# Kernel tuning notes

Measured on AMD Instinct MI355X. Metric: run time of the kernel, lower is better.

Reference implementation:

```python
import jax, jax.numpy as jnp
import numpy as np

LM_TEMP = 2.0      # opts.lm_temp
LAMBDA_SH = 20.0   # lambda_sh passed in ot_loss
EPS = 1e-8


def sinkhorn(M, a, b, lam, num_iter_max=1000, stop_thr=0.005):
    """Faithful port of sinkhorn_pytorch. M:[S,V], a:[S,B], b:[V,B]."""
    K = jnp.exp(-M * lam)          # [S,V]
    KM = K * M
    u0 = jnp.ones_like(a) / a.shape[0]
    v0 = jnp.zeros_like(b)

    def cond(state):
        cpt, u, v, err = state
        return (cpt < num_iter_max) & (err > stop_thr)

    def body(state):
        cpt, u, v, err = state
        u = a / (K @ (b / (u.T @ K).T))   # fused fixed-point step
        cpt = cpt + 1
        do_check = ((cpt % 20) == 1) | (cpt == num_iter_max)

        def check(uve):
            u, v, _ = uve
            v = b / (K.T @ u)
            u = a / (K @ v)
            bb = v * (K.T @ u)
            err = jnp.max(jnp.sum(jnp.abs(bb - b), axis=0))  # inf-norm over batch
            return u, v, err

        u, v, err = jax.lax.cond(do_check, check, lambda t: t, (u, v, err))
        return cpt, u, v, err

    state0 = (jnp.asarray(0, jnp.int32), u0, v0, jnp.asarray(1.0, M.dtype))
    _, u, v, _ = jax.lax.while_loop(cond, body, state0)
    return jnp.sum(u * (KM @ v), axis=0)   # [B] sinkhorn divergences


def setup_inputs() -> dict:
    key = jax.random.key(0)
    ks = jax.random.split(key, 6)
    B, H, V, NV, MAX_SLOTS = 512, 1024, 28996, 3000, 33
    inputs = jax.random.normal(ks[0], (B, 2 * H), jnp.float32)
    outputs = jax.random.normal(ks[1], (B, 512), jnp.float32)
    W_lm = jax.random.normal(ks[2], (V, H), jnp.float32) * 0.02   # lm head (no bias)
    W_lin = jax.random.normal(ks[3], (MAX_SLOTS, 512), jnp.float32) * 0.05
    b_lin = jnp.zeros((MAX_SLOTS,), jnp.float32)
    topics = jax.random.normal(ks[4], (MAX_SLOTS - 1, H), jnp.float32) * 0.01
    verbs = jax.random.randint(ks[5], (NV,), 0, V)
    return {"inputs": inputs, "outputs": outputs, "W_lm": W_lm,
            "W_lin": W_lin, "b_lin": b_lin, "topics": topics,
            "verbs": verbs, "nslots": 33}


def reference(inputs, outputs, W_lm, W_lin, b_lin, topics, verbs, nslots):
    H = W_lm.shape[1]
    # gather verb rows of the lm head once: logits[:, verbs] == x @ W_lm[verbs].T
    W_v = W_lm[verbs]                               # [NV, H]
    Wt = W_v.T                                      # [H, NV]
    o11 = jax.nn.softmax((inputs[:, :H] @ Wt) / LM_TEMP, axis=-1)
    o12 = jax.nn.softmax((inputs[:, H:] @ Wt) / LM_TEMP, axis=-1)
    o1 = (o11 + o12) * 0.5
    o1 = o1 / jnp.sum(o1, axis=1, keepdims=True)    # [B, NV] vocab marginals
    o2 = jax.nn.softmax((outputs @ W_lin.T + b_lin)[:, 1:nslots], axis=-1)  # [B, S]
    # cosine-distance cost matrix between topics and verb embeddings
    tn = topics[:nslots - 1]
    tn = tn / (jnp.linalg.norm(tn, axis=1, keepdims=True) + EPS)
    vn = W_v / (jnp.linalg.norm(W_v, axis=1, keepdims=True) + EPS)
    M = 1.0 - tn @ vn.T                             # [S, NV]
    # single chunk of ot_loss (B <= 1024): mean sinkhorn divergence
    return jnp.mean(sinkhorn(M, o2.T, o1.T, LAMBDA_SH))
```

## Files before the change

kernel.cpp:

```cpp
#include <hip/hip_runtime.h>

#define NV 3000
#define HH 1024
#define BB 512

typedef __attribute__((ext_vector_type(8))) short short8;
typedef __attribute__((ext_vector_type(4))) float floatx4;

__device__ __forceinline__ float wave_sum(float x) {
#pragma unroll
  for (int off = 32; off; off >>= 1) x += __shfl_xor(x, off, 64);
  return x;
}
__device__ __forceinline__ unsigned bf16r(float x) {
  unsigned u = __float_as_uint(x);
  u += 0x7fffu + ((u >> 16) & 1u);
  return u >> 16;
}
__device__ __forceinline__ void gload16(const void* g, void* l) {
  __builtin_amdgcn_global_load_lds(
      (const __attribute__((address_space(1))) unsigned*)g,
      (__attribute__((address_space(3))) unsigned*)l, 16, 0, 0);
}

__global__ __launch_bounds__(256) void norms_wb_kernel(
    const float* __restrict__ W_lm, const float* __restrict__ topics,
    const int* __restrict__ verbs, float* __restrict__ vninv,
    float* __restrict__ tninv, unsigned short* __restrict__ Wb) {
  int r = blockIdx.x, t = threadIdx.x;
  bool isW = r < 3072;
  int j = isW ? (r < NV ? r : NV - 1) : 0;
  const float* src = isW ? (W_lm + (size_t)verbs[j] * HH)
                         : (topics + (size_t)(r - 3072) * HH);
  float4 v = *(const float4*)(src + t * 4);
  if (isW) {
    *(uint2*)(Wb + (size_t)r * HH + t * 4) =
        make_uint2(bf16r(v.x) | (bf16r(v.y) << 16),
                   bf16r(v.z) | (bf16r(v.w) << 16));
  }
  float ss = v.x * v.x + v.y * v.y + v.z * v.z + v.w * v.w;
  ss = wave_sum(ss);
  __shared__ float sq[4];
  if ((t & 63) == 0) sq[t >> 6] = ss;
  __syncthreads();
  if (t == 0) {
    float inv = 1.0f / (sqrtf(sq[0] + sq[1] + sq[2] + sq[3]) + 1e-8f);
    if (isW) { if (r < NV) vninv[r] = inv; }
    else tninv[r - 3072] = inv;
  }
}

__global__ __launch_bounds__(256) void xb_kernel(
    const float* __restrict__ inputs, unsigned short* __restrict__ Xb) {
  int idx = blockIdx.x * 256 + threadIdx.x;
  int r = idx >> 7, c8 = (idx & 127) << 3;
  const float* src = (r < 512) ? (inputs + (size_t)r * 2048 + c8)
                               : (inputs + (size_t)(r - 512) * 2048 + 1024 + c8);
  float4 x0 = ((const float4*)src)[0];
  float4 x1 = ((const float4*)src)[1];
  uint4 o;
  o.x = bf16r(x0.x) | (bf16r(x0.y) << 16);
  o.y = bf16r(x0.z) | (bf16r(x0.w) << 16);
  o.z = bf16r(x1.x) | (bf16r(x1.y) << 16);
  o.w = bf16r(x1.z) | (bf16r(x1.w) << 16);
  *(uint4*)(Xb + (size_t)r * HH + c8) = o;
}

__global__ __launch_bounds__(256) void topt_kernel(
    const float* __restrict__ topics, const float* __restrict__ tninv,
    float* __restrict__ topT) {
  int idx = blockIdx.x * 256 + threadIdx.x;
  int k = idx >> 5, s = idx & 31;
  topT[idx] = topics[(size_t)s * HH + k] * tninv[s];
}

__global__ __launch_bounds__(64) void a_kernel(
    const float* __restrict__ outputs, const float* __restrict__ W_lin,
    const float* __restrict__ b_lin, float* __restrict__ aT) {
  int r = blockIdx.x, t = threadIdx.x;
  __shared__ float orow[512];
  __shared__ float lg[33];
  __shared__ float ms[2];
  *(float4*)(orow + t * 8)     = *(const float4*)(outputs + (size_t)r * 512 + t * 8);
  *(float4*)(orow + t * 8 + 4) = *(const float4*)(outputs + (size_t)r * 512 + t * 8 + 4);
  __syncthreads();
  if (t < 33) {
    float acc = b_lin[t];
    for (int k = 0; k < 512; ++k) acc = fmaf(orow[k], W_lin[(size_t)t * 512 + k], acc);
    lg[t] = acc;
  }
  __syncthreads();
  if (t == 0) {
    float m = lg[1];
    for (int i = 2; i < 33; ++i) m = fmaxf(m, lg[i]);
    float ssum = 0.0f;
    for (int i = 1; i < 33; ++i) ssum += __expf(lg[i] - m);
    ms[0] = m; ms[1] = ssum;
  }
  __syncthreads();
  if (t >= 1 && t < 33) aT[(size_t)r * 32 + t - 1] = __expf(lg[t] - ms[0]) / ms[1];
}

__global__ __launch_bounds__(256) void gemm_mfma(
    const unsigned short* __restrict__ Xb, const unsigned short* __restrict__ Wb,
    float* __restrict__ L) {
  __shared__ unsigned short As[128 * 32], Bs[128 * 32];
  int t = threadIdx.x;
  int wave = t >> 6, ln = t & 63;
  int bn = blockIdx.x, bm = blockIdx.y;
  int wm = (wave >> 1) * 64, wn = (wave & 1) * 64;
  const unsigned short* ga = Xb + (size_t)(bm * 128 + (t >> 2)) * HH + (t & 3) * 8;
  const unsigned short* gb = Wb + (size_t)(bn * 128 + (t >> 2)) * HH + (t & 3) * 8;
  int lq = ln >> 4, lm = ln & 15;
  floatx4 acc[4][4];
#pragma unroll
  for (int i = 0; i < 4; ++i)
#pragma unroll
    for (int j = 0; j < 4; ++j) acc[i][j] = (floatx4)0.0f;

  for (int k0 = 0; k0 < HH; k0 += 32) {
    __syncthreads();
    gload16(ga + k0, As + t * 8);
    gload16(ga + (size_t)64 * HH + k0, As + 2048 + t * 8);
    gload16(gb + k0, Bs + t * 8);
    gload16(gb + (size_t)64 * HH + k0, Bs + 2048 + t * 8);
    __syncthreads();
    short8 af[4], bfr[4];
#pragma unroll
    for (int i = 0; i < 4; ++i)
      af[i] = *(const short8*)(As + (wm + i * 16 + lm) * 32 + lq * 8);
#pragma unroll
    for (int j = 0; j < 4; ++j)
      bfr[j] = *(const short8*)(Bs + (wn + j * 16 + lm) * 32 + lq * 8);
#pragma unroll
    for (int i = 0; i < 4; ++i)
#pragma unroll
      for (int j = 0; j < 4; ++j)
        acc[i][j] = __builtin_amdgcn_mfma_f32_16x16x32_bf16(af[i], bfr[j], acc[i][j], 0, 0, 0);
  }
  int row0 = bm * 128 + wm + lq * 4;
  int col0 = bn * 128 + wn + lm;
#pragma unroll
  for (int j = 0; j < 4; ++j) {
    int col = col0 + j * 16;
    if (col < NV) {
#pragma unroll
      for (int i = 0; i < 4; ++i) {
#pragma unroll
        for (int r = 0; r < 4; ++r)
          L[(size_t)(row0 + i * 16 + r) * NV + col] = acc[i][j][r] * 0.5f;
      }
    }
  }
}

__global__ __launch_bounds__(256) void softmax_kernel(
    float* __restrict__ L1, const float* __restrict__ L2) {
  int r = blockIdx.x, t = threadIdx.x, w = t >> 6, ln = t & 63;
  float* row1 = L1 + (size_t)r * NV;
  const float* row2 = L2 + (size_t)r * NV;
  __shared__ float rd[2][4];
  float s1 = 0.0f, s2 = 0.0f;
  for (int v = t; v < NV; v += 256) { s1 += __expf(row1[v]); s2 += __expf(row2[v]); }
  s1 = wave_sum(s1); s2 = wave_sum(s2);
  if (ln == 0) { rd[0][w] = s1; rd[1][w] = s2; }
  __syncthreads();
  s1 = rd[0][0] + rd[0][1] + rd[0][2] + rd[0][3];
  s2 = rd[1][0] + rd[1][1] + rd[1][2] + rd[1][3];
  float i1 = 0.5f / s1, i2 = 0.5f / s2;
  float rs = 0.0f;
  for (int v = t; v < NV; v += 256) {
    float o = __expf(row1[v]) * i1 + __expf(row2[v]) * i2;
    row1[v] = o; rs += o;
  }
  rs = wave_sum(rs);
  __syncthreads();
  if (ln == 0) rd[0][w] = rs;
  __syncthreads();
  float rinv = 1.0f / (rd[0][0] + rd[0][1] + rd[0][2] + rd[0][3]);
  for (int v = t; v < NV; v += 256) row1[v] *= rinv;
}

__global__ __launch_bounds__(256) void mk_kernel(
    const float* __restrict__ W_lm, const int* __restrict__ verbs,
    const float* __restrict__ topT, const float* __restrict__ vninv,
    unsigned* __restrict__ Kb, float* __restrict__ KMt) {
  __shared__ float red[4][64][33];
  int t = threadIdx.x, ln = t & 63, w = t >> 6;
  int v = blockIdx.x * 64 + ln;
  int vc = v < NV ? v : NV - 1;
  int kb = __builtin_amdgcn_readfirstlane(w) << 8;
  const float* wrow = W_lm + (size_t)verbs[vc] * HH + kb;
  const float* tb = topT + (size_t)kb * 32;
  float acc[32];
#pragma unroll
  for (int s = 0; s < 32; ++s) acc[s] = 0.0f;
  for (int kk = 0; kk < 256; kk += 4) {
    float4 w4 = *(const float4*)(wrow + kk);
    const float* tr = tb + kk * 32;
    const float* pw = (const float*)&w4;
#pragma unroll
    for (int d = 0; d < 4; ++d)
#pragma unroll
      for (int s = 0; s < 32; ++s) acc[s] = fmaf(pw[d], tr[d * 32 + s], acc[s]);
  }
#pragma unroll
  for (int s = 0; s < 32; ++s) red[w][ln][s] = acc[s];
  __syncthreads();
  for (int idx = t; idx < 1024; idx += 256) {
    int l = idx >> 4, pr = idx & 15;
    int vo = blockIdx.x * 64 + l;
    if (vo < NV) {
      int s0 = pr * 2, s1 = s0 + 1;
      float vi = vninv[vo];
      float d0 = red[0][l][s0] + red[1][l][s0] + red[2][l][s0] + red[3][l][s0];
      float d1 = red[0][l][s1] + red[1][l][s1] + red[2][l][s1] + red[3][l][s1];
      float M0 = 1.0f - d0 * vi, M1 = 1.0f - d1 * vi;
      float K0 = __expf(-20.0f * M0), K1 = __expf(-20.0f * M1);
      *(float2*)(KMt + (size_t)vo * 32 + s0) = make_float2(K0 * M0, K1 * M1);
      Kb[(size_t)vo * 16 + pr] = bf16r(K0) | (bf16r(K1) << 16);
    }
  }
}

__device__ __forceinline__ void gridbar(unsigned* bar, unsigned target) {
  __syncthreads();
  if (threadIdx.x == 0) {
    __hip_atomic_fetch_add(bar, 1u, __ATOMIC_RELEASE, __HIP_MEMORY_SCOPE_AGENT);
    while (__hip_atomic_load(bar, __ATOMIC_ACQUIRE, __HIP_MEMORY_SCOPE_AGENT) < target) {
      __builtin_amdgcn_s_sleep(1);
    }
  }
  __syncthreads();
}

#define UNPK(q, o)                                          \
  kc[(o) + 0] = __uint_as_float((q).x << 16);               \
  kc[(o) + 1] = __uint_as_float((q).x & 0xffff0000u);       \
  kc[(o) + 2] = __uint_as_float((q).y << 16);               \
  kc[(o) + 3] = __uint_as_float((q).y & 0xffff0000u);       \
  kc[(o) + 4] = __uint_as_float((q).z << 16);               \
  kc[(o) + 5] = __uint_as_float((q).z & 0xffff0000u);       \
  kc[(o) + 6] = __uint_as_float((q).w << 16);               \
  kc[(o) + 7] = __uint_as_float((q).w & 0xffff0000u);

template <bool STORE_T>
__device__ __forceinline__ void kpass_ss(
    const uint4* __restrict__ Kb, const float* __restrict__ bsh0,
    const float* __restrict__ bsh1, const float* u0, const float* u1,
    float* z0, float* z1, float* vsh0, float* vsh1, int pid, int p) {
#pragma unroll 3
  for (int i = 0; i < 6; ++i) {
    int v = pid + (i << 9);
    if (i < 5 || v < NV) {
      const uint4* kq = Kb + ((size_t)v << 2) + (p << 1);
      uint4 q0 = kq[0], q1 = kq[1];
      float kc[16];
      UNPK(q0, 0) UNPK(q1, 8)
      float w0 = 0.0f, w1 = 0.0f;
#pragma unroll
      for (int s = 0; s < 16; ++s) { w0 = fmaf(kc[s], u0[s], w0); w1 = fmaf(kc[s], u1[s], w1); }
      w0 += __shfl_xor(w0, 1, 64);
      w1 += __shfl_xor(w1, 1, 64);
      float t0 = bsh0[v] * __builtin_amdgcn_rcpf(w0);
      float t1 = bsh1[v] * __builtin_amdgcn_rcpf(w1);
      if (STORE_T && !p) { vsh0[v] = t0; vsh1[v] = t1; }
#pragma unroll
      for (int s = 0; s < 16; ++s) { z0[s] = fmaf(kc[s], t0, z0[s]); z1[s] = fmaf(kc[s], t1, z1[s]); }
    }
  }
}

__device__ __forceinline__ void errpass_ss(
    const uint4* __restrict__ Kb, const float* __restrict__ bsh0,
    const float* __restrict__ bsh1, const float* u0, const float* u1,
    const float* vsh0, const float* vsh1, float& ep0, float& ep1,
    int pid, int p) {
#pragma unroll 3
  for (int i = 0; i < 6; ++i) {
    int v = pid + (i << 9);
    if (i < 5 || v < NV) {
      const uint4* kq = Kb + ((size_t)v << 2) + (p << 1);
      uint4 q0 = kq[0], q1 = kq[1];
      float kc[16];
      UNPK(q0, 0) UNPK(q1, 8)
      float w0 = 0.0f, w1 = 0.0f;
#pragma unroll
      for (int s = 0; s < 16; ++s) { w0 = fmaf(kc[s], u0[s], w0); w1 = fmaf(kc[s], u1[s], w1); }
      w0 += __shfl_xor(w0, 1, 64);
      w1 += __shfl_xor(w1, 1, 64);
      if (!p) {
        ep0 += fabsf(vsh0[v] * w0 - bsh0[v]);
        ep1 += fabsf(vsh1[v] * w1 - bsh1[v]);
      }
    }
  }
}

__device__ __forceinline__ float waveRS16(float* z, int ln) {
  int cnt = 16;
#pragma unroll
  for (int d = 2; d <= 16; d <<= 1) {
    int half = cnt >> 1;
    bool hi = (ln & d) != 0;
#pragma unroll
    for (int k = 0; k < 8; ++k) {
      if (k < half) {
        float a = z[k], b = z[half + k];
        z[k] = hi ? b : a;
        z[half + k] = hi ? a : b;
      }
    }
#pragma unroll
    for (int k = 0; k < 8; ++k)
      if (k < half) z[k] += __shfl_xor(z[half + k], d, 64);
    cnt = half;
  }
  return z[0] + __shfl_xor(z[0], 32, 64);
}

__global__ __launch_bounds__(1024) void sinkhorn_kernel(
    const uint4* __restrict__ Kb, const float* __restrict__ KMt,
    const float* __restrict__ bT, const float* __restrict__ aT,
    unsigned* __restrict__ slots, float* __restrict__ outp) {
  const int t = threadIdx.x;
  const int w = t >> 6, ln = t & 63;
  const int p = t & 1, pid = t >> 1;
  const int col0 = blockIdx.x << 1;
  const float* b0r = bT + (size_t)col0 * NV;
  const float* b1r = b0r + NV;
  float* accres = (float*)(slots + 64);
  unsigned* bar = slots + 65;

  __shared__ float zred[2][16][32];
  __shared__ float ush[2][32];
  __shared__ float sredA[16], sredB[16];
  __shared__ unsigned ebits;
  __shared__ float vsh0[3072], vsh1[3072];
  __shared__ float bsh0[3072], bsh1[3072];
  float* ushf = &ush[0][0];

  const int sl = ((ln & 1) << 4) | ((ln & 2) << 2) | (ln & 4) |
                 ((ln & 8) >> 2) | ((ln & 16) >> 4);

  for (int idx = t; idx < NV; idx += 1024) { bsh0[idx] = b0r[idx]; bsh1[idx] = b1r[idx]; }
  float areg = (t < 64) ? aT[(size_t)col0 * 32 + t] : 0.0f;

  float u0[16], u1[16];
#pragma unroll
  for (int s = 0; s < 16; ++s) { u0[s] = 1.0f / 32.0f; u1[s] = 1.0f / 32.0f; }
  if (t < 64) ushf[t] = 1.0f / 32.0f;
  __syncthreads();
  float err = 1.0f;
  int cpt = 0, chk = 0;
  unsigned barcnt = 0;

  while (cpt < 1000 && err > 0.005f) {
    float z0[16], z1[16];
#pragma unroll
    for (int s = 0; s < 16; ++s) { z0[s] = 0.0f; z1[s] = 0.0f; }
    kpass_ss<false>(Kb, bsh0, bsh1, u0, u1, z0, z1, vsh0, vsh1, pid, p);
    float r0 = waveRS16(z0, ln), r1 = waveRS16(z1, ln);
    __syncthreads();
    if (ln < 32) { zred[0][w][sl] = r0; zred[1][w][sl] = r1; }
    __syncthreads();
    if (t < 64) {
      int c = t >> 5, s = t & 31;
      float zz = 0.0f;
#pragma unroll
      for (int k = 0; k < 16; ++k) zz += zred[c][k][s];
      ushf[t] = areg * __builtin_amdgcn_rcpf(zz);
    }
    __syncthreads();
#pragma unroll
    for (int q = 0; q < 4; ++q) {
      *(float4*)(u0 + q * 4) = *(float4*)(&ush[0][(p << 4) + q * 4]);
      *(float4*)(u1 + q * 4) = *(float4*)(&ush[1][(p << 4) + q * 4]);
    }
    ++cpt;

    if (cpt % 20 == 1 || cpt == 1000) {
#pragma unroll
      for (int s = 0; s < 16; ++s) { z0[s] = 0.0f; z1[s] = 0.0f; }
      kpass_ss<true>(Kb, bsh0, bsh1, u0, u1, z0, z1, vsh0, vsh1, pid, p);
      r0 = waveRS16(z0, ln); r1 = waveRS16(z1, ln);
      __syncthreads();
      if (ln < 32) { zred[0][w][sl] = r0; zred[1][w][sl] = r1; }
      __syncthreads();
      if (t < 64) {
        int c = t >> 5, s = t & 31;
        float zz = 0.0f;
#pragma unroll
        for (int k = 0; k < 16; ++k) zz += zred[c][k][s];
        ushf[t] = areg * __builtin_amdgcn_rcpf(zz);
      }
      __syncthreads();
#pragma unroll
      for (int q = 0; q < 4; ++q) {
        *(float4*)(u0 + q * 4) = *(float4*)(&ush[0][(p << 4) + q * 4]);
        *(float4*)(u1 + q * 4) = *(float4*)(&ush[1][(p << 4) + q * 4]);
      }
      float ep0 = 0.0f, ep1 = 0.0f;
      errpass_ss(Kb, bsh0, bsh1, u0, u1, vsh0, vsh1, ep0, ep1, pid, p);
      ep0 = wave_sum(ep0); ep1 = wave_sum(ep1);
      if (ln == 0) { sredA[w] = ep0; sredB[w] = ep1; }
      __syncthreads();
      if (t == 0) {
        float e0 = 0.0f, e1 = 0.0f;
#pragma unroll
        for (int k = 0; k < 16; ++k) { e0 += sredA[k]; e1 += sredB[k]; }
        atomicMax(slots + chk, __float_as_uint(fmaxf(e0, e1)));
      }
      ++barcnt;
      gridbar(bar, barcnt * 256u);
      if (t == 0) ebits = __hip_atomic_load(slots + chk, __ATOMIC_RELAXED, __HIP_MEMORY_SCOPE_AGENT);
      __syncthreads();
      err = __uint_as_float(ebits);
      ++chk;
    }
  }

  float y0[16], y1[16];
#pragma unroll
  for (int s = 0; s < 16; ++s) { y0[s] = 0.0f; y1[s] = 0.0f; }
#pragma unroll 3
  for (int i = 0; i < 6; ++i) {
    int v = pid + (i << 9);
    if (i < 5 || v < NV) {
      const float4* kp = (const float4*)(KMt + (size_t)v * 32 + (p << 4));
      float kc[16];
#pragma unroll
      for (int q = 0; q < 4; ++q) *(float4*)(kc + q * 4) = kp[q];
      float x0 = vsh0[v], x1 = vsh1[v];
#pragma unroll
      for (int s = 0; s < 16; ++s) { y0[s] = fmaf(kc[s], x0, y0[s]); y1[s] = fmaf(kc[s], x1, y1[s]); }
    }
  }
  float r0 = waveRS16(y0, ln), r1 = waveRS16(y1, ln);
  __syncthreads();
  if (ln < 32) { zred[0][w][sl] = r0; zred[1][w][sl] = r1; }
  __syncthreads();
  if (t < 64) {
    int c = t >> 5, s = t & 31;
    float ys = 0.0f;
#pragma unroll
    for (int k = 0; k < 16; ++k) ys += zred[c][k][s];
    float pp = ys * ushf[t];
#pragma unroll
    for (int off = 1; off <= 16; off <<= 1) pp += __shfl_xor(pp, off, 64);
    float other = __shfl_xor(pp, 32, 64);
    if (t == 0) atomicAdd(accres, pp + other);
  }
  ++barcnt;
  gridbar(bar, barcnt * 256u);
  if (blockIdx.x == 0 && t == 0) {
    unsigned ab = __hip_atomic_load((unsigned*)accres, __ATOMIC_RELAXED, __HIP_MEMORY_SCOPE_AGENT);
    outp[0] = __uint_as_float(ab) / 512.0f;
  }
}

extern "C" void kernel_launch(void* const* d_in, const int* in_sizes, int n_in,
                              void* d_out, int out_size, void* d_ws, size_t ws_size,
                              hipStream_t stream) {
  (void)in_sizes; (void)n_in; (void)out_size; (void)ws_size;
  const float* inputs  = (const float*)d_in[0];
  const float* outputs = (const float*)d_in[1];
  const float* W_lm    = (const float*)d_in[2];
  const float* W_lin   = (const float*)d_in[3];
  const float* b_lin   = (const float*)d_in[4];
  const float* topics  = (const float*)d_in[5];
  const int*   verbs   = (const int*)d_in[6];
  float* out = (float*)d_out;

  char* ws = (char*)d_ws;
  float*    L     = (float*)(ws);
  float*    L1    = L;
  float*    L2    = (float*)(ws + 6144000);
  float*    aT    = (float*)(ws + 12288000);
  unsigned* Kb    = (unsigned*)(ws + 12353536);
  float*    KMt   = (float*)(ws + 12545536);
  float*    topT  = (float*)(ws + 12929536);
  float*    vninv = (float*)(ws + 13060608);
  float*    tninv = (float*)(ws + 13072640);
  unsigned* slots = (unsigned*)(ws + 13072768);
  unsigned short* Xb = (unsigned short*)(ws + 13073280);
  unsigned short* Wb = (unsigned short*)(ws + 15170432);

  hipMemsetAsync((void*)slots, 0, 512, stream);

  norms_wb_kernel<<<3104, 256, 0, stream>>>(W_lm, topics, verbs, vninv, tninv, Wb);
  xb_kernel<<<512, 256, 0, stream>>>(inputs, Xb);
  topt_kernel<<<128, 256, 0, stream>>>(topics, tninv, topT);
  a_kernel<<<BB, 64, 0, stream>>>(outputs, W_lin, b_lin, aT);
  gemm_mfma<<<dim3(24, 8), 256, 0, stream>>>(Xb, Wb, L);
  softmax_kernel<<<BB, 256, 0, stream>>>(L1, L2);
  mk_kernel<<<47, 256, 0, stream>>>(W_lm, verbs, topT, vninv, Kb, KMt);
  sinkhorn_kernel<<<256, 1024, 0, stream>>>((const uint4*)Kb, KMt, L1, aT, slots, out);
}
```

Before: 413.6 us.

## Run Sinkhorn matvecs on bf16 MFMA with split hi/lo vectors

Replaces the scalar FMA K·u and K^T·v passes in the persistent Sinkhorn kernel with 16x16x32 bf16 MFMA instructions. A transposed padded copy of K is added, and the u and v vectors are split into bf16 high and low parts to keep precision close to fp32. The b rows are now read from global memory each iteration instead of being cached in LDS. This aims to cut the vector ALU cost of each iteration, at the cost of extra LDS traffic, more block barriers and some precision risk.

```diff
diff --git a/kernel.cpp b/kernel.cpp
--- a/kernel.cpp
+++ b/kernel.cpp
@@ -184,7 +184,8 @@
 __global__ __launch_bounds__(256) void mk_kernel(
     const float* __restrict__ W_lm, const int* __restrict__ verbs,
     const float* __restrict__ topT, const float* __restrict__ vninv,
-    unsigned* __restrict__ Kb, float* __restrict__ KMt) {
+    unsigned* __restrict__ Kb, unsigned short* __restrict__ KbT,
+    float* __restrict__ KMt) {
   __shared__ float red[4][64][33];
   int t = threadIdx.x, ln = t & 63, w = t >> 6;
   int v = blockIdx.x * 64 + ln;
@@ -210,15 +211,22 @@
   for (int idx = t; idx < 1024; idx += 256) {
     int l = idx >> 4, pr = idx & 15;
     int vo = blockIdx.x * 64 + l;
+    int s0 = pr * 2, s1 = s0 + 1;
     if (vo < NV) {
-      int s0 = pr * 2, s1 = s0 + 1;
       float vi = vninv[vo];
       float d0 = red[0][l][s0] + red[1][l][s0] + red[2][l][s0] + red[3][l][s0];
       float d1 = red[0][l][s1] + red[1][l][s1] + red[2][l][s1] + red[3][l][s1];
       float M0 = 1.0f - d0 * vi, M1 = 1.0f - d1 * vi;
       float K0 = __expf(-20.0f * M0), K1 = __expf(-20.0f * M1);
       *(float2*)(KMt + (size_t)vo * 32 + s0) = make_float2(K0 * M0, K1 * M1);
-      Kb[(size_t)vo * 16 + pr] = bf16r(K0) | (bf16r(K1) << 16);
+      unsigned b0 = bf16r(K0), b1 = bf16r(K1);
+      Kb[(size_t)vo * 16 + pr] = b0 | (b1 << 16);
+      KbT[(size_t)s0 * 3008 + vo] = (unsigned short)b0;
+      KbT[(size_t)s1 * 3008 + vo] = (unsigned short)b1;
+    } else {
+      Kb[(size_t)vo * 16 + pr] = 0u;
+      KbT[(size_t)s0 * 3008 + vo] = 0;
+      KbT[(size_t)s1 * 3008 + vo] = 0;
     }
   }
 }
@@ -232,69 +240,6 @@
     }
   }
   __syncthreads();
-}
-
-#define UNPK(q, o)                                          \
-  kc[(o) + 0] = __uint_as_float((q).x << 16);               \
-  kc[(o) + 1] = __uint_as_float((q).x & 0xffff0000u);       \
-  kc[(o) + 2] = __uint_as_float((q).y << 16);               \
-  kc[(o) + 3] = __uint_as_float((q).y & 0xffff0000u);       \
-  kc[(o) + 4] = __uint_as_float((q).z << 16);               \
-  kc[(o) + 5] = __uint_as_float((q).z & 0xffff0000u);       \
-  kc[(o) + 6] = __uint_as_float((q).w << 16);               \
-  kc[(o) + 7] = __uint_as_float((q).w & 0xffff0000u);
-
-template <bool STORE_T>
-__device__ __forceinline__ void kpass_ss(
-    const uint4* __restrict__ Kb, const float* __restrict__ bsh0,
-    const float* __restrict__ bsh1, const float* u0, const float* u1,
-    float* z0, float* z1, float* vsh0, float* vsh1, int pid, int p) {
-#pragma unroll 3
-  for (int i = 0; i < 6; ++i) {
-    int v = pid + (i << 9);
-    if (i < 5 || v < NV) {
-      const uint4* kq = Kb + ((size_t)v << 2) + (p << 1);
-      uint4 q0 = kq[0], q1 = kq[1];
-      float kc[16];
-      UNPK(q0, 0) UNPK(q1, 8)
-      float w0 = 0.0f, w1 = 0.0f;
-#pragma unroll
-      for (int s = 0; s < 16; ++s) { w0 = fmaf(kc[s], u0[s], w0); w1 = fmaf(kc[s], u1[s], w1); }
-      w0 += __shfl_xor(w0, 1, 64);
-      w1 += __shfl_xor(w1, 1, 64);
-      float t0 = bsh0[v] * __builtin_amdgcn_rcpf(w0);
-      float t1 = bsh1[v] * __builtin_amdgcn_rcpf(w1);
-      if (STORE_T && !p) { vsh0[v] = t0; vsh1[v] = t1; }
-#pragma unroll
-      for (int s = 0; s < 16; ++s) { z0[s] = fmaf(kc[s], t0, z0[s]); z1[s] = fmaf(kc[s], t1, z1[s]); }
-    }
-  }
-}
-
-__device__ __forceinline__ void errpass_ss(
-    const uint4* __restrict__ Kb, const float* __restrict__ bsh0,
-    const float* __restrict__ bsh1, const float* u0, const float* u1,
-    const float* vsh0, const float* vsh1, float& ep0, float& ep1,
-    int pid, int p) {
-#pragma unroll 3
-  for (int i = 0; i < 6; ++i) {
-    int v = pid + (i << 9);
-    if (i < 5 || v < NV) {
-      const uint4* kq = Kb + ((size_t)v << 2) + (p << 1);
-      uint4 q0 = kq[0], q1 = kq[1];
-      float kc[16];
-      UNPK(q0, 0) UNPK(q1, 8)
-      float w0 = 0.0f, w1 = 0.0f;
-#pragma unroll
-      for (int s = 0; s < 16; ++s) { w0 = fmaf(kc[s], u0[s], w0); w1 = fmaf(kc[s], u1[s], w1); }
-      w0 += __shfl_xor(w0, 1, 64);
-      w1 += __shfl_xor(w1, 1, 64);
-      if (!p) {
-        ep0 += fabsf(vsh0[v] * w0 - bsh0[v]);
-        ep1 += fabsf(vsh1[v] * w1 - bsh1[v]);
-      }
-    }
-  }
 }
 
 __device__ __forceinline__ float waveRS16(float* z, int ln) {
@@ -320,11 +265,13 @@
 }
 
 __global__ __launch_bounds__(1024) void sinkhorn_kernel(
-    const uint4* __restrict__ Kb, const float* __restrict__ KMt,
-    const float* __restrict__ bT, const float* __restrict__ aT,
-    unsigned* __restrict__ slots, float* __restrict__ outp) {
+    const unsigned short* __restrict__ Kb, const unsigned short* __restrict__ KbT,
+    const float* __restrict__ KMt, const float* __restrict__ bT,
+    const float* __restrict__ aT, unsigned* __restrict__ slots,
+    float* __restrict__ outp) {
   const int t = threadIdx.x;
-  const int w = t >> 6, ln = t & 63;
+  const int wv = t >> 6, ln = t & 63;
+  const int lm = ln & 15, lq = ln >> 4;
   const int p = t & 1, pid = t >> 1;
   const int col0 = blockIdx.x << 1;
   const float* b0r = bT + (size_t)col0 * NV;
@@ -332,78 +279,149 @@
   float* accres = (float*)(slots + 64);
   unsigned* bar = slots + 65;
 
-  __shared__ float zred[2][16][32];
-  __shared__ float ush[2][32];
+  __shared__ __align__(16) float wshp0[3008], wshp1[3008];
+  __shared__ __align__(16) unsigned short wtbuf[4][3008];
+  __shared__ __align__(16) float zred[16][2][32];
+  __shared__ float ushf[64];
+  __shared__ __align__(16) unsigned short ub[4][32];
   __shared__ float sredA[16], sredB[16];
   __shared__ unsigned ebits;
-  __shared__ float vsh0[3072], vsh1[3072];
-  __shared__ float bsh0[3072], bsh1[3072];
-  float* ushf = &ush[0][0];
+
+  float* wlo0 = (float*)&wtbuf[0][0];
+  float* wlo1 = (float*)&wtbuf[2][0];
+  float* wbase = (lm == 0) ? wshp0 : (lm == 1) ? wshp1 : (lm == 2) ? wlo0 : wlo1;
+  const unsigned short* zbsel = &wtbuf[lm & 3][0];
+  const unsigned short* ubsel = &ub[lm & 3][0];
 
   const int sl = ((ln & 1) << 4) | ((ln & 2) << 2) | (ln & 4) |
                  ((ln & 8) >> 2) | ((ln & 16) >> 4);
 
-  for (int idx = t; idx < NV; idx += 1024) { bsh0[idx] = b0r[idx]; bsh1[idx] = b1r[idx]; }
   float areg = (t < 64) ? aT[(size_t)col0 * 32 + t] : 0.0f;
-
-  float u0[16], u1[16];
-#pragma unroll
-  for (int s = 0; s < 16; ++s) { u0[s] = 1.0f / 32.0f; u1[s] = 1.0f / 32.0f; }
-  if (t < 64) ushf[t] = 1.0f / 32.0f;
-  __syncthreads();
+  if (t < 64) {
+    int c = t >> 5, s = t & 31;
+    ushf[t] = 1.0f / 32.0f;
+    ub[c][s] = (unsigned short)0x3D00u;
+    ub[2 + c][s] = 0;
+  }
+  __syncthreads();
+
   float err = 1.0f;
   int cpt = 0, chk = 0;
   unsigned barcnt = 0;
 
-  while (cpt < 1000 && err > 0.005f) {
-    float z0[16], z1[16];
-#pragma unroll
-    for (int s = 0; s < 16; ++s) { z0[s] = 0.0f; z1[s] = 0.0f; }
-    kpass_ss<false>(Kb, bsh0, bsh1, u0, u1, z0, z1, vsh0, vsh1, pid, p);
-    float r0 = waveRS16(z0, ln), r1 = waveRS16(z1, ln);
-    __syncthreads();
-    if (ln < 32) { zred[0][w][sl] = r0; zred[1][w][sl] = r1; }
+  auto full_iter = [&]() {
+    {
+      short8 bfu = *(const short8*)(ubsel + (lq << 3));
+#pragma unroll
+      for (int i = 0; i < 12; ++i) {
+        int c = wv + (i << 4);
+        if (c < 188) {
+          int v0 = c << 4;
+          short8 af = *(const short8*)(Kb + (size_t)(v0 + lm) * 32 + (lq << 3));
+          floatx4 acc = (floatx4)0.0f;
+          acc = __builtin_amdgcn_mfma_f32_16x16x32_bf16(af, bfu, acc, 0, 0, 0);
+          if (lm < 4) *(floatx4*)(wbase + v0 + (lq << 2)) = acc;
+        }
+      }
+    }
+    __syncthreads();
+    float t0r[3], t1r[3];
+#pragma unroll
+    for (int i = 0; i < 3; ++i) {
+      int v = t + (i << 10);
+      t0r[i] = 0.0f; t1r[i] = 0.0f;
+      if (v < NV) {
+        float w0 = wshp0[v] + wlo0[v];
+        float w1 = wshp1[v] + wlo1[v];
+        t0r[i] = b0r[v] * __builtin_amdgcn_rcpf(w0);
+        t1r[i] = b1r[v] * __builtin_amdgcn_rcpf(w1);
+      }
+    }
+    __syncthreads();
+#pragma unroll
+    for (int i = 0; i < 3; ++i) {
+      int v = t + (i << 10);
+      if (v < 3008) {
+        float T0 = t0r[i], T1 = t1r[i];
+        unsigned h0 = bf16r(T0), h1 = bf16r(T1);
+        wtbuf[0][v] = (unsigned short)h0;
+        wtbuf[1][v] = (unsigned short)h1;
+        wtbuf[2][v] = (unsigned short)bf16r(T0 - __uint_as_float(h0 << 16));
+        wtbuf[3][v] = (unsigned short)bf16r(T1 - __uint_as_float(h1 << 16));
+        wshp0[v] = T0; wshp1[v] = T1;
+      }
+    }
+    __syncthreads();
+    floatx4 accL = (floatx4)0.0f, accH = (floatx4)0.0f;
+#pragma unroll
+    for (int i = 0; i < 6; ++i) {
+      int c = wv + (i << 4);
+      if (c < 94) {
+        int v0 = c << 5;
+        short8 aL = *(const short8*)(KbT + (size_t)lm * 3008 + v0 + (lq << 3));
+        short8 aH = *(const short8*)(KbT + (size_t)(lm + 16) * 3008 + v0 + (lq << 3));
+        short8 bt = *(const short8*)(zbsel + v0 + (lq << 3));
+        accL = __builtin_amdgcn_mfma_f32_16x16x32_bf16(aL, bt, accL, 0, 0, 0);
+        accH = __builtin_amdgcn_mfma_f32_16x16x32_bf16(aH, bt, accH, 0, 0, 0);
+      }
+    }
+    floatx4 zL, zH;
+#pragma unroll
+    for (int r = 0; r < 4; ++r) {
+      zL[r] = accL[r] + __shfl_xor(accL[r], 2, 64);
+      zH[r] = accH[r] + __shfl_xor(accH[r], 2, 64);
+    }
+    if (lm < 2) {
+      *(floatx4*)&zred[wv][lm][lq << 2] = zL;
+      *(floatx4*)&zred[wv][lm][16 + (lq << 2)] = zH;
+    }
     __syncthreads();
     if (t < 64) {
       int c = t >> 5, s = t & 31;
       float zz = 0.0f;
 #pragma unroll
-      for (int k = 0; k < 16; ++k) zz += zred[c][k][s];
-      ushf[t] = areg * __builtin_amdgcn_rcpf(zz);
-    }
-    __syncthreads();
-#pragma unroll
-    for (int q = 0; q < 4; ++q) {
-      *(float4*)(u0 + q * 4) = *(float4*)(&ush[0][(p << 4) + q * 4]);
-      *(float4*)(u1 + q * 4) = *(float4*)(&ush[1][(p << 4) + q * 4]);
-    }
+      for (int k = 0; k < 16; ++k) zz += zred[k][c][s];
+      float uu = areg * __builtin_amdgcn_rcpf(zz);
+      ushf[t] = uu;
+      unsigned h = bf16r(uu);
+      ub[c][s] = (unsigned short)h;
+      ub[2 + c][s] = (unsigned short)bf16r(uu - __uint_as_float(h << 16));
+    }
+    __syncthreads();
+  };
+
+  while (cpt < 1000 && err > 0.005f) {
+    full_iter();
     ++cpt;
-
     if (cpt % 20 == 1 || cpt == 1000) {
-#pragma unroll
-      for (int s = 0; s < 16; ++s) { z0[s] = 0.0f; z1[s] = 0.0f; }
-      kpass_ss<true>(Kb, bsh0, bsh1, u0, u1, z0, z1, vsh0, vsh1, pid, p);
-      r0 = waveRS16(z0, ln); r1 = waveRS16(z1, ln);
-      __syncthreads();
-      if (ln < 32) { zred[0][w][sl] = r0; zred[1][w][sl] = r1; }
-      __syncthreads();
-      if (t < 64) {
-        int c = t >> 5, s = t & 31;
-        float zz = 0.0f;
-#pragma unroll
-        for (int k = 0; k < 16; ++k) zz += zred[c][k][s];
-        ushf[t] = areg * __builtin_amdgcn_rcpf(zz);
-      }
-      __syncthreads();
-#pragma unroll
-      for (int q = 0; q < 4; ++q) {
-        *(float4*)(u0 + q * 4) = *(float4*)(&ush[0][(p << 4) + q * 4]);
-        *(float4*)(u1 + q * 4) = *(float4*)(&ush[1][(p << 4) + q * 4]);
-      }
+      full_iter();
       float ep0 = 0.0f, ep1 = 0.0f;
-      errpass_ss(Kb, bsh0, bsh1, u0, u1, vsh0, vsh1, ep0, ep1, pid, p);
+      {
+        short8 bfu = *(const short8*)(ubsel + (lq << 3));
+#pragma unroll
+        for (int i = 0; i < 12; ++i) {
+          int c = wv + (i << 4);
+          if (c < 188) {
+            int v0 = c << 4;
+            short8 af = *(const short8*)(Kb + (size_t)(v0 + lm) * 32 + (lq << 3));
+            floatx4 acc = (floatx4)0.0f;
+            acc = __builtin_amdgcn_mfma_f32_16x16x32_bf16(af, bfu, acc, 0, 0, 0);
+#pragma unroll
+            for (int r = 0; r < 4; ++r) {
+              float wq = acc[r] + __shfl_xor(acc[r], 2, 64);
+              int v = v0 + (lq << 2) + r;
+              if (lm < 2 && v < NV) {
+                float tt = (lm == 0) ? wshp0[v] : wshp1[v];
+                float bb = (lm == 0) ? b0r[v] : b1r[v];
+                float e = fabsf(tt * wq - bb);
+                if (lm == 0) ep0 += e; else ep1 += e;
+              }
+            }
+          }
+        }
+      }
       ep0 = wave_sum(ep0); ep1 = wave_sum(ep1);
-      if (ln == 0) { sredA[w] = ep0; sredB[w] = ep1; }
+      if (ln == 0) { sredA[wv] = ep0; sredB[wv] = ep1; }
       __syncthreads();
       if (t == 0) {
         float e0 = 0.0f, e1 = 0.0f;
@@ -427,24 +445,24 @@
   for (int i = 0; i < 6; ++i) {
     int v = pid + (i << 9);
     if (i < 5 || v < NV) {
-      const float4* kp = (const float4*)(KMt + (size_t)v * 32 + (p << 4));
+      const floatx4* kp = (const floatx4*)(KMt + (size_t)v * 32 + (p << 4));
       float kc[16];
 #pragma unroll
-      for (int q = 0; q < 4; ++q) *(float4*)(kc + q * 4) = kp[q];
-      float x0 = vsh0[v], x1 = vsh1[v];
+      for (int q = 0; q < 4; ++q) *(floatx4*)(kc + q * 4) = kp[q];
+      float x0 = wshp0[v], x1 = wshp1[v];
 #pragma unroll
       for (int s = 0; s < 16; ++s) { y0[s] = fmaf(kc[s], x0, y0[s]); y1[s] = fmaf(kc[s], x1, y1[s]); }
     }
   }
   float r0 = waveRS16(y0, ln), r1 = waveRS16(y1, ln);
   __syncthreads();
-  if (ln < 32) { zred[0][w][sl] = r0; zred[1][w][sl] = r1; }
+  if (ln < 32) { zred[wv][0][sl] = r0; zred[wv][1][sl] = r1; }
   __syncthreads();
   if (t < 64) {
     int c = t >> 5, s = t & 31;
     float ys = 0.0f;
 #pragma unroll
-    for (int k = 0; k < 16; ++k) ys += zred[c][k][s];
+    for (int k = 0; k < 16; ++k) ys += zred[k][c][s];
     float pp = ys * ushf[t];
 #pragma unroll
     for (int off = 1; off <= 16; off <<= 1) pp += __shfl_xor(pp, off, 64);
@@ -478,13 +496,14 @@
   float*    L2    = (float*)(ws + 6144000);
   float*    aT    = (float*)(ws + 12288000);
   unsigned* Kb    = (unsigned*)(ws + 12353536);
-  float*    KMt   = (float*)(ws + 12545536);
-  float*    topT  = (float*)(ws + 12929536);
-  float*    vninv = (float*)(ws + 13060608);
-  float*    tninv = (float*)(ws + 13072640);
-  unsigned* slots = (unsigned*)(ws + 13072768);
-  unsigned short* Xb = (unsigned short*)(ws + 13073280);
-  unsigned short* Wb = (unsigned short*)(ws + 15170432);
+  float*    KMt   = (float*)(ws + 12546048);
+  float*    topT  = (float*)(ws + 12930048);
+  float*    vninv = (float*)(ws + 13061120);
+  float*    tninv = (float*)(ws + 13073152);
+  unsigned* slots = (unsigned*)(ws + 13073280);
+  unsigned short* Xb  = (unsigned short*)(ws + 13073792);
+  unsigned short* Wb  = (unsigned short*)(ws + 15170944);
+  unsigned short* KbT = (unsigned short*)(ws + 21462400);
 
   hipMemsetAsync((void*)slots, 0, 512, stream);
 
@@ -494,6 +513,7 @@
   a_kernel<<<BB, 64, 0, stream>>>(outputs, W_lin, b_lin, aT);
   gemm_mfma<<<dim3(24, 8), 256, 0, stream>>>(Xb, Wb, L);
   softmax_kernel<<<BB, 256, 0, stream>>>(L1, L2);
-  mk_kernel<<<47, 256, 0, stream>>>(W_lm, verbs, topT, vninv, Kb, KMt);
-  sinkhorn_kernel<<<256, 1024, 0, stream>>>((const uint4*)Kb, KMt, L1, aT, slots, out);
-}
+  mk_kernel<<<47, 256, 0, stream>>>(W_lm, verbs, topT, vninv, Kb, KbT, KMt);
+  sinkhorn_kernel<<<256, 1024, 0, stream>>>((const unsigned short*)Kb, KbT, KMt,
+                                            L1, aT, slots, out);
+}
```

Result: slower. 698.3 us (+68.8%).
